# Kernel tuning notes

Measured on AMD Instinct MI355X. Metric: run time of the kernel, lower is better.

## Reference

```python
import jax, jax.numpy as jnp
import numpy as np

N_NODES = 100000


def _graph_conv(h, src_sl, dst_sl, out_norm, in_norm, W, b):
    # norm='both': h <- D_out^{-1/2} . A . D_in^{-1/2} . h . W + b
    h = h * out_norm[:, None]
    # gather source features over edges, scatter-sum into destinations (SpMM)
    agg = jax.ops.segment_sum(h[src_sl], dst_sl, num_segments=N_NODES)
    agg = agg * in_norm[:, None]
    return agg @ W + b


def setup_inputs() -> dict:
    key = jax.random.key(0)
    ks = jax.random.split(key, 8)
    n_edges = 1600000
    in_feats, n_hidden = 128, 64
    h = jax.random.normal(ks[0], (N_NODES, in_feats), dtype=jnp.float32)
    src = jax.random.randint(ks[1], (n_edges,), 0, N_NODES)
    dst = jax.random.randint(ks[2], (n_edges,), 0, N_NODES)
    dst_node_ids = jax.random.randint(ks[3], (1024,), 0, N_NODES)
    s_in = 1.0 / np.sqrt(in_feats)
    s_h = 1.0 / np.sqrt(n_hidden)
    W0 = jax.random.normal(ks[4], (in_feats, n_hidden), dtype=jnp.float32) * s_in
    W1 = jax.random.normal(ks[5], (n_hidden, n_hidden), dtype=jnp.float32) * s_h
    W2 = jax.random.normal(ks[6], (n_hidden, n_hidden), dtype=jnp.float32) * s_h
    b0 = jnp.zeros((n_hidden,), jnp.float32)
    b1 = jnp.zeros((n_hidden,), jnp.float32)
    b2 = jnp.zeros((n_hidden,), jnp.float32)
    return {"h": h, "src": src, "dst": dst, "dst_node_ids": dst_node_ids,
            "W0": W0, "b0": b0, "W1": W1, "b1": b1, "W2": W2, "b2": b2}


def reference(h, src, dst, dst_node_ids, W0, b0, W1, b1, W2, b2):
    # add_self_loop: append N self edges
    loops = jnp.arange(N_NODES, dtype=src.dtype)
    src_sl = jnp.concatenate([src, loops])
    dst_sl = jnp.concatenate([dst, loops])
    ones = jnp.ones_like(src_sl, dtype=jnp.float32)
    out_deg = jax.ops.segment_sum(ones, src_sl, num_segments=N_NODES)
    in_deg = jax.ops.segment_sum(ones, dst_sl, num_segments=N_NODES)
    out_norm = jax.lax.rsqrt(jnp.maximum(out_deg, 1.0))
    in_norm = jax.lax.rsqrt(jnp.maximum(in_deg, 1.0))
    h = h.astype(jnp.float32)
    # dropout p=0 -> identity between layers
    h = _graph_conv(h, src_sl, dst_sl, out_norm, in_norm, W0, b0)
    h = _graph_conv(h, src_sl, dst_sl, out_norm, in_norm, W1, b1)
    h = _graph_conv(h, src_sl, dst_sl, out_norm, in_norm, W2, b2)
    return h, dst_node_ids
```

## Files before the change

### kernel.cpp

```cpp
#include <hip/hip_runtime.h>

#define N_NODES 100000
#define FOUT 64

#define PSHIFT 9
#define PSIZE  512
#define NPART  ((N_NODES + PSIZE - 1) / PSIZE)
#define TILE   8192
#define SRCBITS 17
#define SRCMASK 0x1FFFF

#define SCAN_BLOCK 256
#define SCAN_ITEMS 8
#define SCAN_ELEMS (SCAN_BLOCK * SCAN_ITEMS)

typedef __attribute__((ext_vector_type(8))) short bf16x8;
typedef __attribute__((ext_vector_type(4))) float f32x4;


static __device__ __forceinline__ float bf2f(unsigned short u) {
    union { unsigned int i; float f; } v;
    v.i = (unsigned int)u << 16;
    return v.f;
}
static __device__ __forceinline__ unsigned short f2bf(float f) {
    union { float f; unsigned int i; } v;
    v.f = f;
    unsigned int r = (v.i + 0x7fffu + ((v.i >> 16) & 1u)) >> 16;
    return (unsigned short)r;
}
static __device__ __forceinline__ float2 up2(unsigned int u) {
    float2 r;
    r.x = bf2f((unsigned short)(u & 0xffffu));
    r.y = bf2f((unsigned short)(u >> 16));
    return r;
}
static __device__ __forceinline__ unsigned int pk2(float x, float y) {
    return (unsigned int)f2bf(x) | ((unsigned int)f2bf(y) << 16);
}

template <typename T> static __device__ __forceinline__ float ldf(const T* p);
template <> __device__ __forceinline__ float ldf<float>(const float* p) { return *p; }
template <> __device__ __forceinline__ float ldf<unsigned short>(const unsigned short* p) { return bf2f(*p); }

template <typename T> static __device__ __forceinline__ void stf(T* p, float v);
template <> __device__ __forceinline__ void stf<float>(float* p, float v) { *p = v; }
template <> __device__ __forceinline__ void stf<unsigned short>(unsigned short* p, float v) { *p = f2bf(v); }

static __device__ __forceinline__ void st2(float* base, int idx, float2 v) {
    ((float2*)base)[idx] = v;
}
static __device__ __forceinline__ void st2(unsigned short* base, int idx, float2 v) {
    ((unsigned int*)base)[idx] = pk2(v.x, v.y);
}


__global__ void k_init(int* __restrict__ dstCnt, int* __restrict__ srcCnt,
                       const int* __restrict__ ids, float* __restrict__ outid, int nid) {
    int i = blockIdx.x * blockDim.x + threadIdx.x;
    if (i < NPART) { dstCnt[i] = 0; srcCnt[i] = 0; }
    if (i < nid) outid[i] = (float)ids[i];
}


__global__ void __launch_bounds__(1024) k_count(
        const int* __restrict__ src, const int* __restrict__ dst,
        int* __restrict__ dstCnt, int* __restrict__ srcCnt, int E) {
    __shared__ int dh[NPART];
    __shared__ int sh2[NPART];
    const int tid = threadIdx.x;
    const int base = blockIdx.x * TILE;
    const int end = min(base + TILE, E);
    if (tid < NPART) { dh[tid] = 0; sh2[tid] = 0; }
    __syncthreads();
    for (int j = base + tid; j < end; j += 1024) {
        atomicAdd(&dh[dst[j] >> PSHIFT], 1);
        atomicAdd(&sh2[src[j] >> PSHIFT], 1);
    }
    __syncthreads();
    if (tid < NPART) {
        if (dh[tid])  atomicAdd(&dstCnt[tid], dh[tid]);
        if (sh2[tid]) atomicAdd(&srcCnt[tid], sh2[tid]);
    }
}

__global__ void k_scan_parts(const int* __restrict__ dstCnt, const int* __restrict__ srcCnt,
                             int* __restrict__ partBaseD, int* __restrict__ partBaseS,
                             int* __restrict__ dstCur, int* __restrict__ srcCur) {
    __shared__ int sb[256];
    const int tid = threadIdx.x;
    int v = (tid < NPART) ? dstCnt[tid] : 0;
    sb[tid] = v;
    __syncthreads();
    for (int off = 1; off < 256; off <<= 1) {
        int x = (tid >= off) ? sb[tid - off] : 0;
        __syncthreads();
        sb[tid] += x;
        __syncthreads();
    }
    int inc = sb[tid];
    if (tid < NPART) {
        partBaseD[tid] = inc - v;
        dstCur[tid]    = inc - v;
        if (tid == NPART - 1) partBaseD[NPART] = inc;
    }
    __syncthreads();
    int v2 = (tid < NPART) ? srcCnt[tid] : 0;
    sb[tid] = v2;
    __syncthreads();
    for (int off = 1; off < 256; off <<= 1) {
        int x = (tid >= off) ? sb[tid - off] : 0;
        __syncthreads();
        sb[tid] += x;
        __syncthreads();
    }
    int inc2 = sb[tid];
    if (tid < NPART) {
        partBaseS[tid] = inc2 - v2;
        srcCur[tid]    = inc2 - v2;
        if (tid == NPART - 1) partBaseS[NPART] = inc2;
    }
}

__global__ void __launch_bounds__(1024) k_binscatter(
        const int* __restrict__ src, const int* __restrict__ dst,
        int* __restrict__ dstCur, int* __restrict__ srcCur,
        unsigned int* __restrict__ dstStream,
        unsigned short* __restrict__ srcStream, int E) {
    __shared__ unsigned int   stageD[TILE];
    __shared__ unsigned short stageS[TILE];
    __shared__ int dh[NPART], sh2[NPART];
    __shared__ int dLoc[NPART], sLoc[NPART];
    __shared__ int dBase[NPART], sBase[NPART];
    __shared__ int dcur[NPART], scur[NPART];
    __shared__ int sbuf[256];

    const int tid = threadIdx.x;
    const int base = blockIdx.x * TILE;
    const int end = min(base + TILE, E);

    if (tid < NPART) { dh[tid] = 0; sh2[tid] = 0; }
    __syncthreads();

    for (int j = base + tid; j < end; j += 1024) {
        atomicAdd(&dh[dst[j] >> PSHIFT], 1);
        atomicAdd(&sh2[src[j] >> PSHIFT], 1);
    }
    __syncthreads();

    {
        int v = 0;
        if (tid < 256) { v = (tid < NPART) ? dh[tid] : 0; sbuf[tid] = v; }
        __syncthreads();
        for (int off = 1; off < 256; off <<= 1) {
            int x = 0;
            if (tid < 256 && tid >= off) x = sbuf[tid - off];
            __syncthreads();
            if (tid < 256) sbuf[tid] += x;
            __syncthreads();
        }
        if (tid < NPART) {
            int inc = sbuf[tid];
            dLoc[tid] = inc - v;
            dcur[tid] = inc - v;
            dBase[tid] = v ? atomicAdd(&dstCur[tid], v) : 0;
        }
        __syncthreads();
    }
    {
        int v = 0;
        if (tid < 256) { v = (tid < NPART) ? sh2[tid] : 0; sbuf[tid] = v; }
        __syncthreads();
        for (int off = 1; off < 256; off <<= 1) {
            int x = 0;
            if (tid < 256 && tid >= off) x = sbuf[tid - off];
            __syncthreads();
            if (tid < 256) sbuf[tid] += x;
            __syncthreads();
        }
        if (tid < NPART) {
            int inc = sbuf[tid];
            sLoc[tid] = inc - v;
            scur[tid] = inc - v;
            sBase[tid] = v ? atomicAdd(&srcCur[tid], v) : 0;
        }
        __syncthreads();
    }

    for (int j = base + tid; j < end; j += 1024) {
        int s = src[j], d = dst[j];
        int pd = atomicAdd(&dcur[d >> PSHIFT], 1);
        stageD[pd] = ((unsigned int)(d & (PSIZE - 1)) << SRCBITS) | (unsigned int)s;
        int ps = atomicAdd(&scur[s >> PSHIFT], 1);
        stageS[ps] = (unsigned short)(s & (PSIZE - 1));
    }
    __syncthreads();

    const int wv = tid >> 6;
    const int lane = tid & 63;
    for (int b = wv; b < NPART; b += 16) {
        const int cnt  = dh[b];
        const int loc  = dLoc[b];
        unsigned int* gd = dstStream + dBase[b];
        for (int i = lane; i < cnt; i += 64) gd[i] = stageD[loc + i];
        const int cnt2 = sh2[b];
        const int loc2 = sLoc[b];
        unsigned short* gs = srcStream + sBase[b];
        for (int i = lane; i < cnt2; i += 64) gs[i] = stageS[loc2 + i];
    }
}

__global__ void k_csr_odeg(const unsigned int* __restrict__ dstStream,
                           const unsigned short* __restrict__ srcStream,
                           const int* __restrict__ partBaseD,
                           const int* __restrict__ partBaseS,
                           int* __restrict__ row_off, int* __restrict__ csr_src,
                           int* __restrict__ out_deg) {
    __shared__ int hist[PSIZE];
    __shared__ int part[PSIZE];
    const int tid = threadIdx.x;

    if (blockIdx.x < NPART) {
        const int p = blockIdx.x;
        const int nodeBase = p << PSHIFT;
        const int nN = min(PSIZE, N_NODES - nodeBase);
        const int e0 = partBaseD[p];
        const int e1 = partBaseD[p + 1];

        for (int i = tid; i < PSIZE; i += 512) hist[i] = 0;
        __syncthreads();
        for (int e = e0 + tid; e < e1; e += 512)
            atomicAdd(&hist[dstStream[e] >> SRCBITS], 1);
        __syncthreads();

        int c = hist[tid];
        part[tid] = c;
        __syncthreads();
        for (int off = 1; off < PSIZE; off <<= 1) {
            int v = (tid >= off) ? part[tid - off] : 0;
            __syncthreads();
            part[tid] += v;
            __syncthreads();
        }
        int run = part[tid] - c;
        hist[tid] = run;
        if (tid < nN) row_off[nodeBase + tid] = e0 + run;
        if (p == NPART - 1 && tid == 0) row_off[N_NODES] = e1;
        __syncthreads();

        for (int e = e0 + tid; e < e1; e += 512) {
            unsigned int rec = dstStream[e];
            int d = rec >> SRCBITS;
            int sv = rec & SRCMASK;
            int pos = atomicAdd(&hist[d], 1);
            csr_src[e0 + pos] = sv;
        }
    } else {
        const int p = blockIdx.x - NPART;
        const int nodeBase = p << PSHIFT;
        const int nN = min(PSIZE, N_NODES - nodeBase);
        const int e0 = partBaseS[p];
        const int e1 = partBaseS[p + 1];

        for (int i = tid; i < PSIZE; i += 512) hist[i] = 0;
        __syncthreads();
        for (int e = e0 + tid; e < e1; e += 512)
            atomicAdd(&hist[srcStream[e]], 1);
        __syncthreads();
        if (tid < nN) out_deg[nodeBase + tid] = hist[tid];
    }
}

template <int FIN, typename TIN, typename TOUT>
__global__ void k_gemm_mfma(const TIN* __restrict__ h, const int* __restrict__ out_deg,
                            const float* __restrict__ W, TOUT* __restrict__ t) {
    constexpr int PITCH = FIN + 8;
    __shared__ unsigned short shA[64 * PITCH];
    __shared__ unsigned short shWt[64 * PITCH];
    __shared__ float sno[64];

    const int tid = threadIdx.x;
    const int row0 = blockIdx.x * 64;

    if (tid < 64) {
        int node = row0 + tid;
        sno[tid] = (node < N_NODES) ? rsqrtf((float)(out_deg[node] + 1)) : 0.f;
    }
    for (int idx = tid; idx < FIN * 64; idx += 256) {
        int k = idx >> 6;
        int nn = idx & 63;
        shWt[nn * PITCH + k] = f2bf(W[idx]);
    }
    __syncthreads();
    for (int idx = tid; idx < 64 * FIN; idx += 256) {
        int r = idx / FIN;
        int c = idx % FIN;
        int node = row0 + r;
        float v = (node < N_NODES) ? ldf(&h[(size_t)node * FIN + c]) * sno[r] : 0.f;
        shA[r * PITCH + c] = f2bf(v);
    }
    __syncthreads();

    const int wv = tid >> 6;
    const int lane = tid & 63;
    const int m = lane & 15;
    const int q = lane >> 4;

    f32x4 acc[4];
#pragma unroll
    for (int i = 0; i < 4; i++) acc[i] = (f32x4){0.f, 0.f, 0.f, 0.f};

    const unsigned short* Arow = &shA[(wv * 16 + m) * PITCH];
#pragma unroll
    for (int kc = 0; kc < FIN / 32; kc++) {
        int kb = kc * 32 + q * 8;
        bf16x8 a = *(const bf16x8*)&Arow[kb];
#pragma unroll
        for (int nt = 0; nt < 4; nt++) {
            bf16x8 b = *(const bf16x8*)&shWt[(nt * 16 + m) * PITCH + kb];
            acc[nt] = __builtin_amdgcn_mfma_f32_16x16x32_bf16(a, b, acc[nt], 0, 0, 0);
        }
    }

#pragma unroll
    for (int nt = 0; nt < 4; nt++) {
#pragma unroll
        for (int i = 0; i < 4; i++) {
            int node = row0 + wv * 16 + q * 4 + i;
            if (node < N_NODES) stf(&t[(size_t)node * FOUT + nt * 16 + m], acc[nt][i]);
        }
    }
}

template <typename TOUT>
__global__ void k_spmm_b(const unsigned int* __restrict__ t2,
                         const int* __restrict__ row_off, const int* __restrict__ csr_src,
                         const float* __restrict__ bias, TOUT* __restrict__ out) {
    const int wave = blockIdx.x * (blockDim.x >> 6) + (threadIdx.x >> 6);
    const int lane = threadIdx.x & 63;
    const int pair = lane >> 5;
    const int c    = lane & 31;
    const int d = wave;
    const int e0 = row_off[d];
    const int deg = row_off[d + 1] - e0;
    const float inorm = rsqrtf((float)(deg + 1));
    const int* bk = csr_src + e0;

    float2 a0 = {0.f, 0.f}, a1 = {0.f, 0.f}, a2 = {0.f, 0.f}, a3 = {0.f, 0.f};
    float2 a4 = {0.f, 0.f}, a5 = {0.f, 0.f}, a6 = {0.f, 0.f}, a7 = {0.f, 0.f};

    if (pair == 0) {
        float2 v = up2(t2[(size_t)d * 32 + c]);
        a0.x += v.x; a0.y += v.y;
    }

    int e = 0;
    for (; e + 16 <= deg; e += 16) {
        int s0 = bk[e + 0  + pair], s1 = bk[e + 2  + pair];
        int s2 = bk[e + 4  + pair], s3 = bk[e + 6  + pair];
        int s4 = bk[e + 8  + pair], s5 = bk[e + 10 + pair];
        int s6 = bk[e + 12 + pair], s7 = bk[e + 14 + pair];
        unsigned int v0 = t2[(size_t)s0 * 32 + c];
        unsigned int v1 = t2[(size_t)s1 * 32 + c];
        unsigned int v2 = t2[(size_t)s2 * 32 + c];
        unsigned int v3 = t2[(size_t)s3 * 32 + c];
        unsigned int v4 = t2[(size_t)s4 * 32 + c];
        unsigned int v5 = t2[(size_t)s5 * 32 + c];
        unsigned int v6 = t2[(size_t)s6 * 32 + c];
        unsigned int v7 = t2[(size_t)s7 * 32 + c];
        float2 f;
        f = up2(v0); a0.x += f.x; a0.y += f.y;
        f = up2(v1); a1.x += f.x; a1.y += f.y;
        f = up2(v2); a2.x += f.x; a2.y += f.y;
        f = up2(v3); a3.x += f.x; a3.y += f.y;
        f = up2(v4); a4.x += f.x; a4.y += f.y;
        f = up2(v5); a5.x += f.x; a5.y += f.y;
        f = up2(v6); a6.x += f.x; a6.y += f.y;
        f = up2(v7); a7.x += f.x; a7.y += f.y;
    }
    for (; e + 8 <= deg; e += 8) {
        int s0 = bk[e + 0 + pair], s1 = bk[e + 2 + pair];
        int s2 = bk[e + 4 + pair], s3 = bk[e + 6 + pair];
        unsigned int v0 = t2[(size_t)s0 * 32 + c];
        unsigned int v1 = t2[(size_t)s1 * 32 + c];
        unsigned int v2 = t2[(size_t)s2 * 32 + c];
        unsigned int v3 = t2[(size_t)s3 * 32 + c];
        float2 f;
        f = up2(v0); a0.x += f.x; a0.y += f.y;
        f = up2(v1); a1.x += f.x; a1.y += f.y;
        f = up2(v2); a2.x += f.x; a2.y += f.y;
        f = up2(v3); a3.x += f.x; a3.y += f.y;
    }
    for (; e + 4 <= deg; e += 4) {
        int s0 = bk[e + 0 + pair], s1 = bk[e + 2 + pair];
        unsigned int v0 = t2[(size_t)s0 * 32 + c];
        unsigned int v1 = t2[(size_t)s1 * 32 + c];
        float2 f;
        f = up2(v0); a0.x += f.x; a0.y += f.y;
        f = up2(v1); a1.x += f.x; a1.y += f.y;
    }
    for (; e + 2 <= deg; e += 2) {
        int s0 = bk[e + pair];
        float2 f = up2(t2[(size_t)s0 * 32 + c]);
        a0.x += f.x; a0.y += f.y;
    }
    if (e < deg && pair == 0) {
        float2 f = up2(t2[(size_t)bk[e] * 32 + c]);
        a0.x += f.x; a0.y += f.y;
    }

    float2 tot;
    tot.x = ((a0.x + a1.x) + (a2.x + a3.x)) + ((a4.x + a5.x) + (a6.x + a7.x));
    tot.y = ((a0.y + a1.y) + (a2.y + a3.y)) + ((a4.y + a5.y) + (a6.y + a7.y));
    tot.x += __shfl_xor(tot.x, 32);
    tot.y += __shfl_xor(tot.y, 32);

    if (pair == 0) {
        float2 bb = *(const float2*)(bias + 2 * c);
        float2 r;
        r.x = inorm * tot.x + bb.x;
        r.y = inorm * tot.y + bb.y;
        st2(out, (int)((size_t)d * 32 + c), r);
    }
}


__global__ void k_init_fb(int* __restrict__ a, int* __restrict__ b,
                          const int* __restrict__ ids, float* __restrict__ outid,
                          int n, int nid) {
    int i = blockIdx.x * blockDim.x + threadIdx.x;
    if (i < n) { a[i] = 0; b[i] = 0; }
    if (i < nid) outid[i] = (float)ids[i];
}

__global__ void k_histo(const int* __restrict__ src, const int* __restrict__ dst,
                        int* __restrict__ out_deg, int* __restrict__ in_deg, int n) {
    int i = blockIdx.x * blockDim.x + threadIdx.x;
    if (i < n) {
        atomicAdd(&out_deg[src[i]], 1);
        atomicAdd(&in_deg[dst[i]], 1);
    }
}

__global__ void k_scan_partial(const int* __restrict__ deg, int* __restrict__ block_sums, int n) {
    __shared__ int red[SCAN_BLOCK];
    const int t = threadIdx.x;
    const int base = blockIdx.x * SCAN_ELEMS + t * SCAN_ITEMS;
    int s = 0;
#pragma unroll
    for (int k = 0; k < SCAN_ITEMS; k++) {
        int i = base + k;
        if (i < n) s += deg[i];
    }
    red[t] = s;
    __syncthreads();
    for (int off = SCAN_BLOCK / 2; off > 0; off >>= 1) {
        if (t < off) red[t] += red[t + off];
        __syncthreads();
    }
    if (t == 0) block_sums[blockIdx.x] = red[0];
}

__global__ void k_scan_blocks(int* __restrict__ block_sums, int nb) {
    __shared__ int sh[SCAN_BLOCK];
    const int t = threadIdx.x;
    sh[t] = (t < nb) ? block_sums[t] : 0;
    __syncthreads();
    for (int off = 1; off < SCAN_BLOCK; off <<= 1) {
        int v = (t >= off) ? sh[t - off] : 0;
        __syncthreads();
        sh[t] += v;
        __syncthreads();
    }
    if (t < nb) block_sums[t] = (t == 0) ? 0 : sh[t - 1];
}

__global__ void k_scan_write(const int* __restrict__ deg, const int* __restrict__ block_off,
                             int* __restrict__ row_off, int* __restrict__ cursor, int n) {
    __shared__ int sh[SCAN_BLOCK];
    const int t = threadIdx.x;
    const int base = blockIdx.x * SCAN_ELEMS + t * SCAN_ITEMS;
    int v[SCAN_ITEMS];
    int s = 0;
#pragma unroll
    for (int k = 0; k < SCAN_ITEMS; k++) {
        int i = base + k;
        v[k] = (i < n) ? deg[i] : 0;
        s += v[k];
    }
    sh[t] = s;
    __syncthreads();
    for (int off = 1; off < SCAN_BLOCK; off <<= 1) {
        int x = (t >= off) ? sh[t - off] : 0;
        __syncthreads();
        sh[t] += x;
        __syncthreads();
    }
    int run = block_off[blockIdx.x] + ((t == 0) ? 0 : sh[t - 1]);
#pragma unroll
    for (int k = 0; k < SCAN_ITEMS; k++) {
        int i = base + k;
        if (i < n) { row_off[i] = run; cursor[i] = run; run += v[k]; }
    }
    if (blockIdx.x == gridDim.x - 1 && t == SCAN_BLOCK - 1) {
        row_off[n] = block_off[blockIdx.x] + sh[SCAN_BLOCK - 1];
    }
}

__global__ void k_scatter(const int* __restrict__ src, const int* __restrict__ dst,
                          int* __restrict__ cursor, int* __restrict__ csr_src, int n) {
    int i = blockIdx.x * blockDim.x + threadIdx.x;
    if (i < n) {
        int d = dst[i];
        int pos = atomicAdd(&cursor[d], 1);
        csr_src[pos] = src[i];
    }
}

template <int FIN>
__global__ void k_gemm_fb(const float* __restrict__ h, const int* __restrict__ out_deg,
                          const float* __restrict__ W, float* __restrict__ t) {
    __shared__ float sh[32 * FIN];
    __shared__ float sno[32];
    const int tid = threadIdx.x;
    const int block0 = blockIdx.x * 32;

    if (tid < 32) sno[tid] = rsqrtf((float)(out_deg[block0 + tid] + 1));
    __syncthreads();

    for (int idx = tid; idx < 32 * FIN; idx += 256) {
        int r = idx / FIN;
        int c = idx % FIN;
        sh[idx] = h[(size_t)(block0 + r) * FIN + c] * sno[r];
    }
    __syncthreads();

    const int j2 = tid & 31;
    const int rg = tid >> 5;
    const float2* W2 = (const float2*)W;
    float2 a0 = {0.f, 0.f}, a1 = {0.f, 0.f}, a2 = {0.f, 0.f}, a3 = {0.f, 0.f};
#pragma unroll 4
    for (int k = 0; k < FIN; k++) {
        float2 w = W2[k * 32 + j2];
        float s0 = sh[(rg + 0)  * FIN + k];
        float s1 = sh[(rg + 8)  * FIN + k];
        float s2 = sh[(rg + 16) * FIN + k];
        float s3 = sh[(rg + 24) * FIN + k];
        a0.x += s0 * w.x; a0.y += s0 * w.y;
        a1.x += s1 * w.x; a1.y += s1 * w.y;
        a2.x += s2 * w.x; a2.y += s2 * w.y;
        a3.x += s3 * w.x; a3.y += s3 * w.y;
    }
    float* tp = t + (size_t)block0 * FOUT;
    st2(tp, (rg + 0)  * 32 + j2, a0);
    st2(tp, (rg + 8)  * 32 + j2, a1);
    st2(tp, (rg + 16) * 32 + j2, a2);
    st2(tp, (rg + 24) * 32 + j2, a3);
}

__global__ void k_spmm_c(const float* __restrict__ t, const int* __restrict__ row_off,
                         const int* __restrict__ csr_src, const float* __restrict__ bias,
                         float* __restrict__ out) {
    const int wave = blockIdx.x * (blockDim.x >> 6) + (threadIdx.x >> 6);
    const int lane = threadIdx.x & 63;
    const int d = wave;
    const int e0 = row_off[d];
    const int e1 = row_off[d + 1];
    const float inorm = rsqrtf((float)(e1 - e0 + 1));

    float a0 = t[(size_t)d * FOUT + lane];
    float a1 = 0.f, a2 = 0.f, a3 = 0.f, a4 = 0.f, a5 = 0.f, a6 = 0.f, a7 = 0.f;
    int e = e0;
    for (; e + 8 <= e1; e += 8) {
        int s0 = csr_src[e + 0], s1 = csr_src[e + 1], s2 = csr_src[e + 2], s3 = csr_src[e + 3];
        int s4 = csr_src[e + 4], s5 = csr_src[e + 5], s6 = csr_src[e + 6], s7 = csr_src[e + 7];
        a0 += t[(size_t)s0 * FOUT + lane];
        a1 += t[(size_t)s1 * FOUT + lane];
        a2 += t[(size_t)s2 * FOUT + lane];
        a3 += t[(size_t)s3 * FOUT + lane];
        a4 += t[(size_t)s4 * FOUT + lane];
        a5 += t[(size_t)s5 * FOUT + lane];
        a6 += t[(size_t)s6 * FOUT + lane];
        a7 += t[(size_t)s7 * FOUT + lane];
    }
    for (; e + 4 <= e1; e += 4) {
        int s0 = csr_src[e + 0], s1 = csr_src[e + 1], s2 = csr_src[e + 2], s3 = csr_src[e + 3];
        a0 += t[(size_t)s0 * FOUT + lane];
        a1 += t[(size_t)s1 * FOUT + lane];
        a2 += t[(size_t)s2 * FOUT + lane];
        a3 += t[(size_t)s3 * FOUT + lane];
    }
    for (; e < e1; e++) a0 += t[(size_t)csr_src[e] * FOUT + lane];

    float acc = ((a0 + a1) + (a2 + a3)) + ((a4 + a5) + (a6 + a7));
    out[(size_t)d * FOUT + lane] = inorm * acc + bias[lane];
}


extern "C" void kernel_launch(void* const* d_in, const int* in_sizes, int n_in,
                              void* d_out, int out_size, void* d_ws, size_t ws_size,
                              hipStream_t stream) {
    const float* h   = (const float*)d_in[0];
    const int*   src = (const int*)d_in[1];
    const int*   dst = (const int*)d_in[2];
    const int*   ids = (const int*)d_in[3];
    const float* W0  = (const float*)d_in[4];
    const float* b0  = (const float*)d_in[5];
    const float* W1  = (const float*)d_in[6];
    const float* b1  = (const float*)d_in[7];
    const float* W2  = (const float*)d_in[8];
    const float* b2  = (const float*)d_in[9];
    const int N = N_NODES;
    const int E = in_sizes[1];

    size_t o = 0;
    auto alloc = [&](size_t nbytes) -> void* {
        void* p = (char*)d_ws + o;
        o += (nbytes + 255) & ~(size_t)255;
        return p;
    };

    float* outp = (float*)d_out;
    const int B = 256;
    const int spmmGrid = N / 4;
    const int mfmaGrid = (N + 63) / 64;

    const size_t needNew =
        (((size_t)E * 4 + 255) & ~(size_t)255) +
        (((size_t)E * 2 + 255) & ~(size_t)255) +
        (((size_t)E * 4 + 255) & ~(size_t)255) +
        (((size_t)(N + 1) * 4 + 255) & ~(size_t)255) +
        (((size_t)N * 4 + 255) & ~(size_t)255) +
        6 * 1024 +
        2 * (((size_t)N * FOUT * 2 + 255) & ~(size_t)255) + 4096;

    if (ws_size >= needNew) {
        unsigned int*   dstStream = (unsigned int*)alloc((size_t)E * 4);
        unsigned short* srcStream = (unsigned short*)alloc((size_t)E * 2);
        int*            csr_src   = (int*)alloc((size_t)E * 4);
        int*            row_off   = (int*)alloc((size_t)(N + 1) * 4);
        int*            out_deg   = (int*)alloc((size_t)N * 4);
        int*            dstCnt    = (int*)alloc(1024);
        int*            srcCnt    = (int*)alloc(1024);
        int*            dstCur    = (int*)alloc(1024);
        int*            srcCur    = (int*)alloc(1024);
        int*            partBaseD = (int*)alloc(1024);
        int*            partBaseS = (int*)alloc(1024);
        unsigned short* t         = (unsigned short*)alloc((size_t)N * FOUT * 2);
        unsigned short* hbuf      = (unsigned short*)alloc((size_t)N * FOUT * 2);

        const int nTiles = (E + TILE - 1) / TILE;

        k_init<<<4, B, 0, stream>>>(dstCnt, srcCnt, ids, outp + (size_t)N * FOUT, 1024);
        k_count<<<nTiles, 1024, 0, stream>>>(src, dst, dstCnt, srcCnt, E);
        k_scan_parts<<<1, 256, 0, stream>>>(dstCnt, srcCnt, partBaseD, partBaseS, dstCur, srcCur);
        k_binscatter<<<nTiles, 1024, 0, stream>>>(src, dst, dstCur, srcCur, dstStream, srcStream, E);
        k_csr_odeg<<<2 * NPART, 512, 0, stream>>>(dstStream, srcStream, partBaseD, partBaseS,
                                                  row_off, csr_src, out_deg);

        k_gemm_mfma<128, float, unsigned short><<<mfmaGrid, 256, 0, stream>>>(h, out_deg, W0, t);
        k_spmm_b<unsigned short><<<spmmGrid, 256, 0, stream>>>((const unsigned int*)t, row_off, csr_src, b0, hbuf);
        k_gemm_mfma<64, unsigned short, unsigned short><<<mfmaGrid, 256, 0, stream>>>(hbuf, out_deg, W1, t);
        k_spmm_b<unsigned short><<<spmmGrid, 256, 0, stream>>>((const unsigned int*)t, row_off, csr_src, b1, hbuf);
        k_gemm_mfma<64, unsigned short, unsigned short><<<mfmaGrid, 256, 0, stream>>>(hbuf, out_deg, W2, t);
        k_spmm_b<float><<<spmmGrid, 256, 0, stream>>>((const unsigned int*)t, row_off, csr_src, b2, outp);
    } else {
        int*   in_deg  = (int*)alloc((size_t)N * 4);
        int*   out_deg = (int*)alloc((size_t)N * 4);
        int*   row_off = (int*)alloc((size_t)(N + 1) * 4);
        int*   cursor  = (int*)alloc((size_t)N * 4);
        int*   csr_src = (int*)alloc((size_t)E * 4);
        float* t       = (float*)alloc((size_t)N * FOUT * 4);
        float* hbuf    = (float*)alloc((size_t)N * FOUT * 4);
        int*   bsums   = (int*)alloc((size_t)SCAN_BLOCK * 4);

        const int gN = (N + B - 1) / B;
        const int gE = (E + B - 1) / B;
        const int nScanBlocks = (N + SCAN_ELEMS - 1) / SCAN_ELEMS;

        k_init_fb<<<gN, B, 0, stream>>>(in_deg, out_deg, ids, outp + (size_t)N * FOUT, N, 1024);
        k_histo<<<gE, B, 0, stream>>>(src, dst, out_deg, in_deg, E);
        k_scan_partial<<<nScanBlocks, SCAN_BLOCK, 0, stream>>>(in_deg, bsums, N);
        k_scan_blocks<<<1, SCAN_BLOCK, 0, stream>>>(bsums, nScanBlocks);
        k_scan_write<<<nScanBlocks, SCAN_BLOCK, 0, stream>>>(in_deg, bsums, row_off, cursor, N);
        k_scatter<<<gE, B, 0, stream>>>(src, dst, cursor, csr_src, E);

        k_gemm_fb<128><<<N / 32, 256, 0, stream>>>(h, out_deg, W0, t);
        k_spmm_c<<<spmmGrid, 256, 0, stream>>>(t, row_off, csr_src, b0, hbuf);
        k_gemm_fb<64><<<N / 32, 256, 0, stream>>>(hbuf, out_deg, W1, t);
        k_spmm_c<<<spmmGrid, 256, 0, stream>>>(t, row_off, csr_src, b1, hbuf);
        k_gemm_fb<64><<<N / 32, 256, 0, stream>>>(hbuf, out_deg, W2, t);
        k_spmm_c<<<spmmGrid, 256, 0, stream>>>(t, row_off, csr_src, b2, outp);
    }
}
```

Before: 361.8 us.

## Keep weight fragments in registers for GEMM and widen SpMM gathers to four-edge lanes

Weights are pre-transposed to bf16 once in a new prep kernel. The GEMM is rewritten so each wave keeps its B fragments in registers and loads A rows directly from global memory, with no shared-memory staging. The out-degree normalization moves to the output, where it scales the accumulators. The SpMM is restructured so each wave processes four edges at a time, with 16 lanes each gathering 8-byte chunks. It folds the self-loop into the tail iteration and reduces the partial sums by shuffle. The intent is to remove shared-memory round trips and the per-block weight conversion, and to cut loop overhead in the gather. The risks are lower memory-level parallelism per wave in the SpMM and uncoalesced direct global A loads.

```diff
diff --git a/kernel.cpp b/kernel.cpp
--- a/kernel.cpp
+++ b/kernel.cpp
@@ -39,10 +39,6 @@
     return (unsigned int)f2bf(x) | ((unsigned int)f2bf(y) << 16);
 }
 
-template <typename T> static __device__ __forceinline__ float ldf(const T* p);
-template <> __device__ __forceinline__ float ldf<float>(const float* p) { return *p; }
-template <> __device__ __forceinline__ float ldf<unsigned short>(const unsigned short* p) { return bf2f(*p); }
-
 template <typename T> static __device__ __forceinline__ void stf(T* p, float v);
 template <> __device__ __forceinline__ void stf<float>(float* p, float v) { *p = v; }
 template <> __device__ __forceinline__ void stf<unsigned short>(unsigned short* p, float v) { *p = f2bf(v); }
@@ -52,6 +48,31 @@
 }
 static __device__ __forceinline__ void st2(unsigned short* base, int idx, float2 v) {
     ((unsigned int*)base)[idx] = pk2(v.x, v.y);
+}
+
+static __device__ __forceinline__ void st4(float* base, size_t idx, float4 v) {
+    ((float4*)base)[idx] = v;
+}
+static __device__ __forceinline__ void st4(unsigned short* base, size_t idx, float4 v) {
+    uint2 u;
+    u.x = pk2(v.x, v.y);
+    u.y = pk2(v.z, v.w);
+    ((uint2*)base)[idx] = u;
+}
+
+template <typename TIN> static __device__ __forceinline__ bf16x8 ldA(const TIN* p);
+template <> __device__ __forceinline__ bf16x8 ldA<unsigned short>(const unsigned short* p) {
+    return *(const bf16x8*)p;
+}
+template <> __device__ __forceinline__ bf16x8 ldA<float>(const float* p) {
+    const f32x4* q = (const f32x4*)p;
+    f32x4 lo = q[0], hi = q[1];
+    bf16x8 a;
+    a[0] = (short)f2bf(lo[0]); a[1] = (short)f2bf(lo[1]);
+    a[2] = (short)f2bf(lo[2]); a[3] = (short)f2bf(lo[3]);
+    a[4] = (short)f2bf(hi[0]); a[5] = (short)f2bf(hi[1]);
+    a[6] = (short)f2bf(hi[2]); a[7] = (short)f2bf(hi[3]);
+    return a;
 }
 
 
@@ -60,6 +81,22 @@
     int i = blockIdx.x * blockDim.x + threadIdx.x;
     if (i < NPART) { dstCnt[i] = 0; srcCnt[i] = 0; }
     if (i < nid) outid[i] = (float)ids[i];
+}
+
+__global__ void k_prepW(const float* __restrict__ W0, const float* __restrict__ W1,
+                        const float* __restrict__ W2,
+                        unsigned short* __restrict__ Wt0, unsigned short* __restrict__ Wt1,
+                        unsigned short* __restrict__ Wt2) {
+    int i = blockIdx.x * blockDim.x + threadIdx.x;
+    if (i < 128 * 64) {
+        int k = i >> 6, n = i & 63;
+        Wt0[n * 128 + k] = f2bf(W0[i]);
+    }
+    if (i < 64 * 64) {
+        int k = i >> 6, n = i & 63;
+        Wt1[n * 64 + k] = f2bf(W1[i]);
+        Wt2[n * 64 + k] = f2bf(W2[i]);
+    }
 }
 
 
@@ -272,155 +309,98 @@
 }
 
 template <int FIN, typename TIN, typename TOUT>
-__global__ void k_gemm_mfma(const TIN* __restrict__ h, const int* __restrict__ out_deg,
-                            const float* __restrict__ W, TOUT* __restrict__ t) {
-    constexpr int PITCH = FIN + 8;
-    __shared__ unsigned short shA[64 * PITCH];
-    __shared__ unsigned short shWt[64 * PITCH];
-    __shared__ float sno[64];
-
-    const int tid = threadIdx.x;
-    const int row0 = blockIdx.x * 64;
-
-    if (tid < 64) {
-        int node = row0 + tid;
-        sno[tid] = (node < N_NODES) ? rsqrtf((float)(out_deg[node] + 1)) : 0.f;
-    }
-    for (int idx = tid; idx < FIN * 64; idx += 256) {
-        int k = idx >> 6;
-        int nn = idx & 63;
-        shWt[nn * PITCH + k] = f2bf(W[idx]);
-    }
-    __syncthreads();
-    for (int idx = tid; idx < 64 * FIN; idx += 256) {
-        int r = idx / FIN;
-        int c = idx % FIN;
-        int node = row0 + r;
-        float v = (node < N_NODES) ? ldf(&h[(size_t)node * FIN + c]) * sno[r] : 0.f;
-        shA[r * PITCH + c] = f2bf(v);
-    }
-    __syncthreads();
-
-    const int wv = tid >> 6;
-    const int lane = tid & 63;
+__global__ void k_gemm_reg(const TIN* __restrict__ h, const int* __restrict__ out_deg,
+                           const unsigned short* __restrict__ Wt, TOUT* __restrict__ t) {
+    constexpr int NKC = FIN / 32;
+    const int lane = threadIdx.x & 63;
     const int m = lane & 15;
     const int q = lane >> 4;
-
-    f32x4 acc[4];
-#pragma unroll
-    for (int i = 0; i < 4; i++) acc[i] = (f32x4){0.f, 0.f, 0.f, 0.f};
-
-    const unsigned short* Arow = &shA[(wv * 16 + m) * PITCH];
-#pragma unroll
-    for (int kc = 0; kc < FIN / 32; kc++) {
-        int kb = kc * 32 + q * 8;
-        bf16x8 a = *(const bf16x8*)&Arow[kb];
+    const int wid = blockIdx.x * (blockDim.x >> 6) + (threadIdx.x >> 6);
+    const int nw = (gridDim.x * blockDim.x) >> 6;
+    const int nTiles = N_NODES / 16;
+
+    bf16x8 bfrag[NKC][4];
+#pragma unroll
+    for (int kc = 0; kc < NKC; kc++)
+#pragma unroll
+        for (int nt = 0; nt < 4; nt++)
+            bfrag[kc][nt] = *(const bf16x8*)&Wt[(nt * 16 + m) * FIN + kc * 32 + q * 8];
+
+    for (int tile = wid; tile < nTiles; tile += nw) {
+        const TIN* hrow = h + (size_t)(tile * 16 + m) * FIN + q * 8;
+        f32x4 acc[4];
+#pragma unroll
+        for (int nt = 0; nt < 4; nt++) acc[nt] = (f32x4){0.f, 0.f, 0.f, 0.f};
+#pragma unroll
+        for (int kc = 0; kc < NKC; kc++) {
+            bf16x8 a = ldA(hrow + kc * 32);
+#pragma unroll
+            for (int nt = 0; nt < 4; nt++)
+                acc[nt] = __builtin_amdgcn_mfma_f32_16x16x32_bf16(a, bfrag[kc][nt], acc[nt], 0, 0, 0);
+        }
+        const int r0 = tile * 16 + q * 4;
+        int4 dg = *(const int4*)&out_deg[r0];
+        float s0 = rsqrtf((float)(dg.x + 1));
+        float s1 = rsqrtf((float)(dg.y + 1));
+        float s2 = rsqrtf((float)(dg.z + 1));
+        float s3 = rsqrtf((float)(dg.w + 1));
 #pragma unroll
         for (int nt = 0; nt < 4; nt++) {
-            bf16x8 b = *(const bf16x8*)&shWt[(nt * 16 + m) * PITCH + kb];
-            acc[nt] = __builtin_amdgcn_mfma_f32_16x16x32_bf16(a, b, acc[nt], 0, 0, 0);
-        }
-    }
-
-#pragma unroll
-    for (int nt = 0; nt < 4; nt++) {
-#pragma unroll
-        for (int i = 0; i < 4; i++) {
-            int node = row0 + wv * 16 + q * 4 + i;
-            if (node < N_NODES) stf(&t[(size_t)node * FOUT + nt * 16 + m], acc[nt][i]);
+            TOUT* tp = t + (size_t)r0 * FOUT + nt * 16 + m;
+            stf(tp + 0 * FOUT, acc[nt][0] * s0);
+            stf(tp + 1 * FOUT, acc[nt][1] * s1);
+            stf(tp + 2 * FOUT, acc[nt][2] * s2);
+            stf(tp + 3 * FOUT, acc[nt][3] * s3);
         }
     }
 }
 
 template <typename TOUT>
-__global__ void k_spmm_b(const unsigned int* __restrict__ t2,
+__global__ void k_spmm_b(const uint2* __restrict__ t2,
                          const int* __restrict__ row_off, const int* __restrict__ csr_src,
                          const float* __restrict__ bias, TOUT* __restrict__ out) {
     const int wave = blockIdx.x * (blockDim.x >> 6) + (threadIdx.x >> 6);
     const int lane = threadIdx.x & 63;
-    const int pair = lane >> 5;
-    const int c    = lane & 31;
+    const int sub = lane >> 4;
+    const int c2 = lane & 15;
     const int d = wave;
     const int e0 = row_off[d];
     const int deg = row_off[d + 1] - e0;
     const float inorm = rsqrtf((float)(deg + 1));
     const int* bk = csr_src + e0;
 
-    float2 a0 = {0.f, 0.f}, a1 = {0.f, 0.f}, a2 = {0.f, 0.f}, a3 = {0.f, 0.f};
-    float2 a4 = {0.f, 0.f}, a5 = {0.f, 0.f}, a6 = {0.f, 0.f}, a7 = {0.f, 0.f};
-
-    if (pair == 0) {
-        float2 v = up2(t2[(size_t)d * 32 + c]);
-        a0.x += v.x; a0.y += v.y;
-    }
-
-    int e = 0;
-    for (; e + 16 <= deg; e += 16) {
-        int s0 = bk[e + 0  + pair], s1 = bk[e + 2  + pair];
-        int s2 = bk[e + 4  + pair], s3 = bk[e + 6  + pair];
-        int s4 = bk[e + 8  + pair], s5 = bk[e + 10 + pair];
-        int s6 = bk[e + 12 + pair], s7 = bk[e + 14 + pair];
-        unsigned int v0 = t2[(size_t)s0 * 32 + c];
-        unsigned int v1 = t2[(size_t)s1 * 32 + c];
-        unsigned int v2 = t2[(size_t)s2 * 32 + c];
-        unsigned int v3 = t2[(size_t)s3 * 32 + c];
-        unsigned int v4 = t2[(size_t)s4 * 32 + c];
-        unsigned int v5 = t2[(size_t)s5 * 32 + c];
-        unsigned int v6 = t2[(size_t)s6 * 32 + c];
-        unsigned int v7 = t2[(size_t)s7 * 32 + c];
-        float2 f;
-        f = up2(v0); a0.x += f.x; a0.y += f.y;
-        f = up2(v1); a1.x += f.x; a1.y += f.y;
-        f = up2(v2); a2.x += f.x; a2.y += f.y;
-        f = up2(v3); a3.x += f.x; a3.y += f.y;
-        f = up2(v4); a4.x += f.x; a4.y += f.y;
-        f = up2(v5); a5.x += f.x; a5.y += f.y;
-        f = up2(v6); a6.x += f.x; a6.y += f.y;
-        f = up2(v7); a7.x += f.x; a7.y += f.y;
-    }
-    for (; e + 8 <= deg; e += 8) {
-        int s0 = bk[e + 0 + pair], s1 = bk[e + 2 + pair];
-        int s2 = bk[e + 4 + pair], s3 = bk[e + 6 + pair];
-        unsigned int v0 = t2[(size_t)s0 * 32 + c];
-        unsigned int v1 = t2[(size_t)s1 * 32 + c];
-        unsigned int v2 = t2[(size_t)s2 * 32 + c];
-        unsigned int v3 = t2[(size_t)s3 * 32 + c];
-        float2 f;
-        f = up2(v0); a0.x += f.x; a0.y += f.y;
-        f = up2(v1); a1.x += f.x; a1.y += f.y;
-        f = up2(v2); a2.x += f.x; a2.y += f.y;
-        f = up2(v3); a3.x += f.x; a3.y += f.y;
-    }
-    for (; e + 4 <= deg; e += 4) {
-        int s0 = bk[e + 0 + pair], s1 = bk[e + 2 + pair];
-        unsigned int v0 = t2[(size_t)s0 * 32 + c];
-        unsigned int v1 = t2[(size_t)s1 * 32 + c];
-        float2 f;
-        f = up2(v0); a0.x += f.x; a0.y += f.y;
-        f = up2(v1); a1.x += f.x; a1.y += f.y;
-    }
-    for (; e + 2 <= deg; e += 2) {
-        int s0 = bk[e + pair];
-        float2 f = up2(t2[(size_t)s0 * 32 + c]);
-        a0.x += f.x; a0.y += f.y;
-    }
-    if (e < deg && pair == 0) {
-        float2 f = up2(t2[(size_t)bk[e] * 32 + c]);
-        a0.x += f.x; a0.y += f.y;
-    }
-
-    float2 tot;
-    tot.x = ((a0.x + a1.x) + (a2.x + a3.x)) + ((a4.x + a5.x) + (a6.x + a7.x));
-    tot.y = ((a0.y + a1.y) + (a2.y + a3.y)) + ((a4.y + a5.y) + (a6.y + a7.y));
-    tot.x += __shfl_xor(tot.x, 32);
-    tot.y += __shfl_xor(tot.y, 32);
-
-    if (pair == 0) {
-        float2 bb = *(const float2*)(bias + 2 * c);
-        float2 r;
-        r.x = inorm * tot.x + bb.x;
-        r.y = inorm * tot.y + bb.y;
-        st2(out, (int)((size_t)d * 32 + c), r);
+    float4 acc = {0.f, 0.f, 0.f, 0.f};
+    const int nFull = deg >> 2;
+    for (int it = 0; it < nFull; ++it) {
+        int s = bk[it * 4 + sub];
+        uint2 v = t2[(size_t)s * 16 + c2];
+        float2 f0 = up2(v.x), f1 = up2(v.y);
+        acc.x += f0.x; acc.y += f0.y; acc.z += f1.x; acc.w += f1.y;
+    }
+    {
+        int idx = nFull * 4 + sub;
+        int s = (idx < deg) ? bk[idx] : d;
+        float sc = (idx <= deg) ? 1.f : 0.f;
+        uint2 v = t2[(size_t)s * 16 + c2];
+        float2 f0 = up2(v.x), f1 = up2(v.y);
+        acc.x = fmaf(sc, f0.x, acc.x);
+        acc.y = fmaf(sc, f0.y, acc.y);
+        acc.z = fmaf(sc, f1.x, acc.z);
+        acc.w = fmaf(sc, f1.y, acc.w);
+    }
+    acc.x += __shfl_xor(acc.x, 16); acc.y += __shfl_xor(acc.y, 16);
+    acc.z += __shfl_xor(acc.z, 16); acc.w += __shfl_xor(acc.w, 16);
+    acc.x += __shfl_xor(acc.x, 32); acc.y += __shfl_xor(acc.y, 32);
+    acc.z += __shfl_xor(acc.z, 32); acc.w += __shfl_xor(acc.w, 32);
+
+    if (sub == 0) {
+        float4 bb = *(const float4*)(bias + 4 * c2);
+        float4 r;
+        r.x = inorm * acc.x + bb.x;
+        r.y = inorm * acc.y + bb.y;
+        r.z = inorm * acc.z + bb.z;
+        r.w = inorm * acc.w + bb.w;
+        st4(out, (size_t)d * 16 + c2, r);
     }
 }
 
@@ -623,7 +603,7 @@
     float* outp = (float*)d_out;
     const int B = 256;
     const int spmmGrid = N / 4;
-    const int mfmaGrid = (N + 63) / 64;
+    const int gemmGrid = (N / 16 + 3) / 4;
 
     const size_t needNew =
         (((size_t)E * 4 + 255) & ~(size_t)255) +
@@ -632,7 +612,8 @@
         (((size_t)(N + 1) * 4 + 255) & ~(size_t)255) +
         (((size_t)N * 4 + 255) & ~(size_t)255) +
         6 * 1024 +
-        2 * (((size_t)N * FOUT * 2 + 255) & ~(size_t)255) + 4096;
+        2 * (((size_t)N * FOUT * 2 + 255) & ~(size_t)255) +
+        64 * 1024 + 4096;
 
     if (ws_size >= needNew) {
         unsigned int*   dstStream = (unsigned int*)alloc((size_t)E * 4);
@@ -648,22 +629,26 @@
         int*            partBaseS = (int*)alloc(1024);
         unsigned short* t         = (unsigned short*)alloc((size_t)N * FOUT * 2);
         unsigned short* hbuf      = (unsigned short*)alloc((size_t)N * FOUT * 2);
+        unsigned short* Wt0       = (unsigned short*)alloc(128 * 64 * 2);
+        unsigned short* Wt1       = (unsigned short*)alloc(64 * 64 * 2);
+        unsigned short* Wt2       = (unsigned short*)alloc(64 * 64 * 2);
 
         const int nTiles = (E + TILE - 1) / TILE;
 
         k_init<<<4, B, 0, stream>>>(dstCnt, srcCnt, ids, outp + (size_t)N * FOUT, 1024);
+        k_prepW<<<32, B, 0, stream>>>(W0, W1, W2, Wt0, Wt1, Wt2);
         k_count<<<nTiles, 1024, 0, stream>>>(src, dst, dstCnt, srcCnt, E);
         k_scan_parts<<<1, 256, 0, stream>>>(dstCnt, srcCnt, partBaseD, partBaseS, dstCur, srcCur);
         k_binscatter<<<nTiles, 1024, 0, stream>>>(src, dst, dstCur, srcCur, dstStream, srcStream, E);
         k_csr_odeg<<<2 * NPART, 512, 0, stream>>>(dstStream, srcStream, partBaseD, partBaseS,
                                                   row_off, csr_src, out_deg);
 
-        k_gemm_mfma<128, float, unsigned short><<<mfmaGrid, 256, 0, stream>>>(h, out_deg, W0, t);
-        k_spmm_b<unsigned short><<<spmmGrid, 256, 0, stream>>>((const unsigned int*)t, row_off, csr_src, b0, hbuf);
-        k_gemm_mfma<64, unsigned short, unsigned short><<<mfmaGrid, 256, 0, stream>>>(hbuf, out_deg, W1, t);
-        k_spmm_b<unsigned short><<<spmmGrid, 256, 0, stream>>>((const unsigned int*)t, row_off, csr_src, b1, hbuf);
-        k_gemm_mfma<64, unsigned short, unsigned short><<<mfmaGrid, 256, 0, stream>>>(hbuf, out_deg, W2, t);
-        k_spmm_b<float><<<spmmGrid, 256, 0, stream>>>((const unsigned int*)t, row_off, csr_src, b2, outp);
+        k_gemm_reg<128, float, unsigned short><<<gemmGrid, B, 0, stream>>>(h, out_deg, Wt0, t);
+        k_spmm_b<unsigned short><<<spmmGrid, B, 0, stream>>>((const uint2*)t, row_off, csr_src, b0, hbuf);
+        k_gemm_reg<64, unsigned short, unsigned short><<<gemmGrid, B, 0, stream>>>(hbuf, out_deg, Wt1, t);
+        k_spmm_b<unsigned short><<<spmmGrid, B, 0, stream>>>((const uint2*)t, row_off, csr_src, b1, hbuf);
+        k_gemm_reg<64, unsigned short, unsigned short><<<gemmGrid, B, 0, stream>>>(hbuf, out_deg, Wt2, t);
+        k_spmm_b<float><<<spmmGrid, B, 0, stream>>>((const uint2*)t, row_off, csr_src, b2, outp);
     } else {
         int*   in_deg  = (int*)alloc((size_t)N * 4);
         int*   out_deg = (int*)alloc((size_t)N * 4);
```

Result: slower. 380.2 us (+5.1%).
